# Kernel optimization log

Hardware: AMD Instinct MI355X
Metric: run time of the kernel (lower is better)

The kernel has to match this reference:

```python
import jax, jax.numpy as jnp
import numpy as np

WIN = 8
HEADS = 8
DOWN = 4
STRIDE = WIN // DOWN  # 2
LEVELS = len([i for i in range(8) if WIN / DOWN**i >= 1])  # 2
EPS = 1e-5


def circular_pad(x, pad_r, pad_b):
    # x: (N, H, W, C) -> (N, H+pad_b, W+pad_r, C), circular repeat like torch repeat+slice
    N, H, W, C = x.shape
    Hr = -(-(H + pad_b) // H)
    Wr = -(-(W + pad_r) // W)
    return jnp.tile(x, (1, Hr, Wr, 1))[:, :H + pad_b, :W + pad_r, :]


def pad_fit_win(x, ws):
    N, H, W, C = x.shape
    H_ = -(-H // ws) * ws
    W_ = -(-W // ws) * ws
    return circular_pad(x, W_ - W, H_ - H)


def window_partition(x, ws):
    N, H, W, C = x.shape
    x = x.reshape(N, H // ws, ws, W // ws, ws, C)
    return x.transpose(0, 1, 3, 2, 4, 5).reshape(-1, ws, ws, C)


def window_reverse(w, ws, H, W):
    B = w.shape[0] // ((H // ws) * (W // ws))
    x = w.reshape(B, H // ws, W // ws, ws, ws, -1)
    return x.transpose(0, 1, 3, 2, 4, 5).reshape(B, H, W, -1)


def layernorm(x, g, b):
    mu = jnp.mean(x, -1, keepdims=True)
    var = jnp.var(x, -1, keepdims=True)
    return (x - mu) * jax.lax.rsqrt(var + EPS) * g + b


def mha(q, k, v, wq, wk, wv, wf, bf):
    # q: (B, Lq, C); k, v: (B, Lk, C). Weights stored as (in, out); eval mode (no dropout).
    B, Lq, C = q.shape
    Lk = k.shape[1]
    dh = C // HEADS
    qh = (q @ wq).reshape(B, Lq, HEADS, dh)
    kh = (k @ wk).reshape(B, Lk, HEADS, dh)
    vh = (v @ wv).reshape(B, Lk, HEADS, dh)
    attn = jnp.einsum('bqhd,bkhd->bhqk', qh, kh) * (1.0 / dh ** 0.5)
    attn = jax.nn.softmax(attn, axis=-1)
    o = jnp.einsum('bhqk,bkhd->bqhd', attn, vh).reshape(B, Lq, C)
    return o @ wf + bf


def self_attention(x, wq, wk, wv, wf, bf):
    N, H, W, C = x.shape
    xp = pad_fit_win(x, WIN)
    _, H_, W_, _ = xp.shape
    xw = window_partition(xp, WIN).reshape(-1, WIN * WIN, C)
    res = mha(xw, xw, xw, wq, wk, wv, wf, bf)
    res = window_reverse(res.reshape(-1, WIN, WIN, C), WIN, H_, W_)
    return (xp + res)[:, :H, :W, :]


def cross_attention(q, kv, wq, wk, wv, wf, bf):
    # q: (N,qH,qW,C) non-overlapping windows; kv: (N,kH,kW,C) overlapping unfold windows
    N, qH, qW, C = q.shape
    _, kH, kW, _ = kv.shape
    qp = pad_fit_win(q, WIN)
    _, qH_, qW_, _ = qp.shape
    qw = window_partition(qp, WIN).reshape(-1, WIN * WIN, C)
    kH_ = (-(-kH // STRIDE) - 1) * STRIDE + WIN
    kW_ = (-(-kW // STRIDE) - 1) * STRIDE + WIN
    kvp = circular_pad(kv, kW_ - kW, kH_ - kH)
    nH = (kH_ - WIN) // STRIDE + 1
    nW = (kW_ - WIN) // STRIDE + 1
    ri = (jnp.arange(nH) * STRIDE)[:, None] + jnp.arange(WIN)
    ci = (jnp.arange(nW) * STRIDE)[:, None] + jnp.arange(WIN)
    patches = kvp[:, ri][:, :, :, ci]
    patches = patches.transpose(0, 1, 3, 2, 4, 5).reshape(-1, WIN * WIN, C)
    res = mha(qw, patches, patches, wq, wk, wv, wf, bf)
    res = window_reverse(res.reshape(-1, WIN, WIN, C), WIN, qH_, qW_)
    return (qp + res)[:, :qH, :qW, :]


def avgpool4(x):  # NHWC avg pool with kernel=stride=DOWN
    N, H, W, C = x.shape
    return x.reshape(N, H // DOWN, DOWN, W // DOWN, DOWN, C).mean((2, 4))


def setup_inputs() -> dict:
    key = jax.random.key(0)
    ks = jax.random.split(key, 12)
    D, DF = 256, 1024
    N, H, W = 8, 128, 128
    s = 0.02

    def w(k, shape):
        return jax.random.normal(k, shape, jnp.float32) * s

    return {
        'x': jax.random.normal(ks[0], (N, D, H, W), jnp.float32),
        'sa_wq': w(ks[1], (D, D)), 'sa_wk': w(ks[2], (D, D)), 'sa_wv': w(ks[3], (D, D)),
        'sa_wf': w(ks[4], (D, D)), 'sa_bf': jnp.zeros((D,), jnp.float32),
        'ca_wq': w(ks[5], (D, D)), 'ca_wk': w(ks[6], (D, D)), 'ca_wv': w(ks[7], (D, D)),
        'ca_wf': w(ks[8], (D, D)), 'ca_bf': jnp.zeros((D,), jnp.float32),
        'ln_self_g': jnp.ones((D,), jnp.float32), 'ln_self_b': jnp.zeros((D,), jnp.float32),
        'ln_cross_g': jnp.ones((D,), jnp.float32), 'ln_cross_b': jnp.zeros((D,), jnp.float32),
        'ffn_w1': w(ks[9], (D, DF)), 'ffn_b1': jnp.zeros((DF,), jnp.float32),
        'ffn_w2': w(ks[10], (DF, D)), 'ffn_b2': jnp.zeros((D,), jnp.float32),
        'ln_out_g': jnp.ones((D,), jnp.float32), 'ln_out_b': jnp.zeros((D,), jnp.float32),
    }


def reference(x, sa_wq, sa_wk, sa_wv, sa_wf, sa_bf,
              ca_wq, ca_wk, ca_wv, ca_wf, ca_bf,
              ln_self_g, ln_self_b, ln_cross_g, ln_cross_b,
              ffn_w1, ffn_b1, ffn_w2, ffn_b2, ln_out_g, ln_out_b):
    N, C, H, W = x.shape
    xh = x.transpose(0, 2, 3, 1)  # NHWC
    xh = pad_fit_win(xh, WIN)
    attn_list = []
    for idx in range(LEVELS):
        xa = self_attention(xh, sa_wq, sa_wk, sa_wv, sa_wf, sa_bf)
        xa = layernorm(xa, ln_self_g, ln_self_b)
        attn_list.append(xa)
        if idx < LEVELS - 1:
            xh = avgpool4(xa)
    kv = attn_list[-1]
    for idx in range(LEVELS - 1, 0, -1):
        q = cross_attention(attn_list[idx - 1], kv, ca_wq, ca_wk, ca_wv, ca_wf, ca_bf)
        q = layernorm(q, ln_cross_g, ln_cross_b)
        kv = q
    q = kv[:, :H, :W, :]
    res = jax.nn.relu(q @ ffn_w1 + ffn_b1) @ ffn_w2 + ffn_b2
    out = layernorm(q + res, ln_out_g, ln_out_b)
    return out.transpose(0, 3, 1, 2)
```

## Files before the change

kernel.cpp:

```cpp
#include <hip/hip_runtime.h>

typedef _Float16 h16;
typedef _Float16 f16x8 __attribute__((ext_vector_type(8)));
typedef _Float16 f16x4 __attribute__((ext_vector_type(4)));
typedef float f32x4 __attribute__((ext_vector_type(4)));

__device__ __forceinline__ float b2f(h16 v){ return (float)v; }
__device__ __forceinline__ h16 f2b(float v){ return (h16)v; }

#define CDIM 256
#define NHEADS 8
#define DH 32

__global__ __launch_bounds__(256) void k_wt_all(const float* __restrict__ s0, const float* __restrict__ s1,
                                                const float* __restrict__ s2, const float* __restrict__ s3,
                                                const float* __restrict__ s4, const float* __restrict__ s5,
                                                const float* __restrict__ s6, const float* __restrict__ s7,
                                                const float* __restrict__ s8, const float* __restrict__ s9,
                                                h16* __restrict__ wsc)
{
    __shared__ float T[32][33];
    int b = blockIdx.x;
    const float* src; h16* dst; int K, N, ti, tj;
    if (b < 512) {
        int w = b >> 6, rem = b & 63;
        ti = rem >> 3; tj = rem & 7; K = 256; N = 256;
        switch (w) {
            case 0: src = s0; break; case 1: src = s1; break;
            case 2: src = s2; break; case 3: src = s3; break;
            case 4: src = s4; break; case 5: src = s5; break;
            case 6: src = s6; break; default: src = s7; break;
        }
        dst = wsc + w * 65536;
    } else if (b < 768) {
        int rem = b - 512; ti = rem >> 5; tj = rem & 31; K = 256; N = 1024;
        src = s8; dst = wsc + 8 * 65536;
    } else {
        int rem = b - 768; ti = rem >> 3; tj = rem & 7; K = 1024; N = 256;
        src = s9; dst = wsc + 8 * 65536 + 262144;
    }
    int rr = threadIdx.x >> 5, c = threadIdx.x & 31;
    #pragma unroll
    for (int i = 0; i < 4; ++i) {
        int r = i * 8 + rr;
        T[r][c] = src[(long long)(ti * 32 + r) * N + tj * 32 + c];
    }
    __syncthreads();
    #pragma unroll
    for (int i = 0; i < 4; ++i) {
        int r = i * 8 + rr;
        dst[(long long)(tj * 32 + r) * K + ti * 32 + c] = f2b(T[c][r]);
    }
}

__global__ __launch_bounds__(256) void k_nchw2nhwc(const float* __restrict__ x, h16* __restrict__ o,
                                                   int Hh, int Ww)
{
    __shared__ float T[64][65];
    int bid = blockIdx.x;
    int cb = bid & 3; bid >>= 2;
    int nwb = Ww >> 6;
    int wb = bid % nwb; bid /= nwb;
    int h = bid % Hh;
    int n = bid / Hh;
    int lane = threadIdx.x & 63, grp = threadIdx.x >> 6;
    int w0 = wb << 6;
    long long HW = (long long)Hh * Ww;
    long long rbase = ((long long)(n * CDIM + cb * 64) * Hh + h) * Ww + w0;
    #pragma unroll
    for (int i = 0; i < 16; ++i) {
        int cl = grp * 16 + i;
        T[cl][lane] = x[rbase + (long long)cl * HW + lane];
    }
    __syncthreads();
    long long obase = (long long)(n * Hh + h) * Ww + w0;
    #pragma unroll
    for (int i = 0; i < 16; ++i) {
        int wl = grp * 16 + i;
        o[(obase + wl) * CDIM + cb * 64 + lane] = f2b(T[lane][wl]);
    }
}

__global__ __launch_bounds__(256) void k_gemm_mfma(const h16* __restrict__ A, const h16* __restrict__ Bt,
                                                   const float* __restrict__ bias, const h16* __restrict__ Cadd,
                                                   h16* __restrict__ C,
                                                   int M, int N, int K, int ldbt, int ldc,
                                                   long long ostride, int relu)
{
    __shared__ __align__(16) h16 As[128 * 64];
    __shared__ __align__(16) h16 Bs[128 * 64];
    const int tid = threadIdx.x;
    const int wave = tid >> 6, lane = tid & 63;
    const int row0 = blockIdx.y * 128, col0 = blockIdx.x * 128;
    const int wm = (wave >> 1) * 64, wn = (wave & 1) * 64;

    f32x4 acc[4][4] = {};

    const int srow = wave * 32 + (lane >> 3);
    const int skel = (lane & 7) * 8;
    const h16* ag = A  + (long long)(row0 + srow) * K    + skel;
    const h16* bg = Bt + (long long)(col0 + srow) * ldbt + skel;
    h16* as_base = As + (wave * 32) * 64;
    h16* bs_base = Bs + (wave * 32) * 64;

    for (int k0 = 0; k0 < K; k0 += 64) {
        #pragma unroll
        for (int i = 0; i < 4; ++i) {
            __builtin_amdgcn_global_load_lds(
                (const __attribute__((address_space(1))) void*)(ag + (long long)i * 8 * K),
                (__attribute__((address_space(3))) void*)(as_base + i * 8 * 64), 16, 0, 0);
            __builtin_amdgcn_global_load_lds(
                (const __attribute__((address_space(1))) void*)(bg + (long long)i * 8 * ldbt),
                (__attribute__((address_space(3))) void*)(bs_base + i * 8 * 64), 16, 0, 0);
        }
        ag += 64; bg += 64;
        __syncthreads();
        #pragma unroll
        for (int kk = 0; kk < 2; ++kk) {
            const int ko = kk * 32 + (lane >> 4) * 8;
            f16x8 af[4], bb[4];
            #pragma unroll
            for (int i = 0; i < 4; ++i) {
                af[i] = *(const f16x8*)(As + (wm + i * 16 + (lane & 15)) * 64 + ko);
                bb[i] = *(const f16x8*)(Bs + (wn + i * 16 + (lane & 15)) * 64 + ko);
            }
            #pragma unroll
            for (int i = 0; i < 4; ++i)
                #pragma unroll
                for (int j = 0; j < 4; ++j)
                    acc[i][j] = __builtin_amdgcn_mfma_f32_16x16x32_f16(af[i], bb[j], acc[i][j], 0, 0, 0);
        }
        __syncthreads();
    }

    const int cr = (lane >> 4) * 4;
    const int cc = lane & 15;
    #pragma unroll
    for (int j = 0; j < 4; ++j) {
        int col = col0 + wn + j * 16 + cc;
        int grp = col >> 8;
        long long cb = (long long)grp * ostride + (col & 255);
        float bv = bias ? bias[col] : 0.f;
        #pragma unroll
        for (int i = 0; i < 4; ++i) {
            #pragma unroll
            for (int r = 0; r < 4; ++r) {
                long long row = row0 + wm + i * 16 + cr + r;
                float v = acc[i][j][r] + bv;
                if (relu) v = fmaxf(v, 0.f);
                long long addr = cb + row * ldc;
                if (Cadd) v += b2f(Cadd[addr]);
                C[addr] = f2b(v);
            }
        }
    }
}

__global__ __launch_bounds__(256) void k_attn_mfma(const h16* __restrict__ Q, const h16* __restrict__ Kp,
                                                   const h16* __restrict__ Vp, h16* __restrict__ O,
                                                   int Hh, int Ww, int cross)
{
    __shared__ __align__(16) h16 SpA[4][64 * 64];
    __shared__ __align__(16) h16 VtA[4][32 * 64];
    const int tid = threadIdx.x;
    const int wave = tid >> 6, lane = tid & 63;
    const int l15 = lane & 15, g = lane >> 4;
    h16* Sp = SpA[wave];
    h16* Vt = VtA[wave];

    const int win = blockIdx.x;
    int n, wi, wj;
    if (cross) { n = win >> 8; wi = (win >> 4) & 15; wj = win & 15; }
    else {
        int nw = Ww >> 3, nh = Hh >> 3;
        n = win / (nh * nw);
        int rem = win - n * (nh * nw);
        wi = rem / nw; wj = rem - (rem / nw) * nw;
    }
    auto qtok = [&](int t) {
        return cross ? (n * 128 + wi * 8 + (t >> 3)) * 128 + wj * 8 + (t & 7)
                     : (n * Hh + wi * 8 + (t >> 3)) * Ww + wj * 8 + (t & 7);
    };
    auto ktok = [&](int t) {
        return cross ? (n * 32 + ((wi * 2 + (t >> 3)) & 31)) * 32 + ((wj * 2 + (t & 7)) & 31)
                     : qtok(t);
    };
    const float scale = 0.17677669529663687f;

    int qt_frag[4], kt_frag[4];
    #pragma unroll
    for (int i = 0; i < 4; ++i) { qt_frag[i] = qtok(i * 16 + l15); kt_frag[i] = ktok(i * 16 + l15); }
    const int vtok = ktok(lane);
    int otok[4][4];
    #pragma unroll
    for (int qt = 0; qt < 4; ++qt)
        #pragma unroll
        for (int rr = 0; rr < 4; ++rr)
            otok[qt][rr] = qtok(qt * 16 + g * 4 + rr);

    #pragma unroll 1
    for (int hh = 0; hh < 2; ++hh) {
        const int h = wave * 2 + hh;
        const int hoff = h * 32;

        f16x8 vin[4];
        #pragma unroll
        for (int j = 0; j < 4; ++j)
            vin[j] = *(const f16x8*)(Vp + (long long)vtok * CDIM + hoff + j * 8);

        f16x8 kf[4], qf[4];
        #pragma unroll
        for (int i = 0; i < 4; ++i) {
            kf[i] = *(const f16x8*)(Kp + (long long)kt_frag[i] * CDIM + hoff + g * 8);
            qf[i] = *(const f16x8*)(Q  + (long long)qt_frag[i] * CDIM + hoff + g * 8);
        }

        #pragma unroll
        for (int j = 0; j < 4; ++j)
            #pragma unroll
            for (int e = 0; e < 8; ++e) {
                int d = j * 8 + e;
                Vt[(d * 64 + lane) ^ ((d & 7) << 3)] = vin[j][e];
            }

        f32x4 sT[4][4] = {};
        #pragma unroll
        for (int i = 0; i < 4; ++i)
            #pragma unroll
            for (int jq = 0; jq < 4; ++jq)
                sT[i][jq] = __builtin_amdgcn_mfma_f32_16x16x32_f16(kf[i], qf[jq], sT[i][jq], 0, 0, 0);

        #pragma unroll
        for (int jq = 0; jq < 4; ++jq) {
            float m = -1e30f;
            #pragma unroll
            for (int i = 0; i < 4; ++i)
                #pragma unroll
                for (int rr = 0; rr < 4; ++rr)
                    m = fmaxf(m, sT[i][jq][rr]);
            m = fmaxf(m, __shfl_xor(m, 16));
            m = fmaxf(m, __shfl_xor(m, 32));
            float p[16];
            float sum = 0.f;
            #pragma unroll
            for (int i = 0; i < 4; ++i)
                #pragma unroll
                for (int rr = 0; rr < 4; ++rr) {
                    float e = __expf((sT[i][jq][rr] - m) * scale);
                    p[i * 4 + rr] = e; sum += e;
                }
            sum += __shfl_xor(sum, 16);
            sum += __shfl_xor(sum, 32);
            float inv = 1.f / sum;
            int q = jq * 16 + l15;
            int rowbase = q * 64, swz = (q & 7) << 3;
            #pragma unroll
            for (int i = 0; i < 4; ++i) {
                f16x4 pk;
                pk[0] = (h16)(p[i * 4 + 0] * inv);
                pk[1] = (h16)(p[i * 4 + 1] * inv);
                pk[2] = (h16)(p[i * 4 + 2] * inv);
                pk[3] = (h16)(p[i * 4 + 3] * inv);
                *(f16x4*)(Sp + ((rowbase + i * 16 + g * 4) ^ swz)) = pk;
            }
        }
        asm volatile("s_waitcnt lgkmcnt(0)" ::: "memory");

        f32x4 o[4][2] = {};
        #pragma unroll
        for (int kb = 0; kb < 2; ++kb) {
            f16x8 vb[2];
            #pragma unroll
            for (int dt = 0; dt < 2; ++dt) {
                int d = dt * 16 + l15;
                vb[dt] = *(const f16x8*)(Vt + ((d * 64 + kb * 32 + g * 8) ^ ((d & 7) << 3)));
            }
            #pragma unroll
            for (int qt = 0; qt < 4; ++qt) {
                int q = qt * 16 + l15;
                f16x8 pa = *(const f16x8*)(Sp + ((q * 64 + kb * 32 + g * 8) ^ ((q & 7) << 3)));
                #pragma unroll
                for (int dt = 0; dt < 2; ++dt)
                    o[qt][dt] = __builtin_amdgcn_mfma_f32_16x16x32_f16(pa, vb[dt], o[qt][dt], 0, 0, 0);
            }
        }

        #pragma unroll
        for (int qt = 0; qt < 4; ++qt)
            #pragma unroll
            for (int rr = 0; rr < 4; ++rr) {
                long long tb = (long long)otok[qt][rr] * CDIM + hoff;
                #pragma unroll
                for (int dt = 0; dt < 2; ++dt)
                    O[tb + dt * 16 + l15] = f2b(o[qt][dt][rr]);
            }
        asm volatile("s_waitcnt lgkmcnt(0)" ::: "memory");
    }
}

__global__ __launch_bounds__(256) void k_ln(const h16* __restrict__ A, const h16* __restrict__ Bb,
                                            const float* __restrict__ g, const float* __restrict__ be,
                                            h16* __restrict__ O)
{
    int tid = threadIdx.x;
    int t = tid >> 5;
    int j = tid & 31;
    long long base = ((long long)blockIdx.x * 8 + t) * CDIM + j * 8;
    f16x8 a = *(const f16x8*)(A + base);
    f16x8 b = *(const f16x8*)(Bb + base);
    float v[8]; float s = 0.f, s2 = 0.f;
    #pragma unroll
    for (int e = 0; e < 8; ++e) { float vv = b2f(a[e]) + b2f(b[e]); v[e] = vv; s += vv; s2 += vv * vv; }
    #pragma unroll
    for (int off = 1; off < 32; off <<= 1) { s += __shfl_xor(s, off); s2 += __shfl_xor(s2, off); }
    float mu = s * (1.f / 256.f);
    float inv = rsqrtf(s2 * (1.f / 256.f) - mu * mu + 1e-5f);
    f32x4 g0 = *(const f32x4*)(g + j * 8),  g1 = *(const f32x4*)(g + j * 8 + 4);
    f32x4 e0 = *(const f32x4*)(be + j * 8), e1 = *(const f32x4*)(be + j * 8 + 4);
    f16x8 y;
    #pragma unroll
    for (int e = 0; e < 4; ++e) y[e] = f2b((v[e] - mu) * inv * g0[e] + e0[e]);
    #pragma unroll
    for (int e = 0; e < 4; ++e) y[e + 4] = f2b((v[e + 4] - mu) * inv * g1[e] + e1[e]);
    *(f16x8*)(O + base) = y;
}

__global__ __launch_bounds__(256) void k_ln_out(const h16* __restrict__ A, const h16* __restrict__ Bb,
                                                const float* __restrict__ g, const float* __restrict__ be,
                                                float* __restrict__ O, int HW)
{
    __shared__ float Y[32][257];
    int tid = threadIdx.x;
    int t = tid >> 5;
    int j = tid & 31;
    long long tok0 = (long long)blockIdx.x * 32;
    f32x4 g0 = *(const f32x4*)(g + j * 8),  g1 = *(const f32x4*)(g + j * 8 + 4);
    f32x4 e0 = *(const f32x4*)(be + j * 8), e1 = *(const f32x4*)(be + j * 8 + 4);
    #pragma unroll
    for (int pass = 0; pass < 4; ++pass) {
        int ta = pass * 8 + t;
        long long base = (tok0 + ta) * CDIM + j * 8;
        f16x8 a = *(const f16x8*)(A + base);
        f16x8 b = *(const f16x8*)(Bb + base);
        float v[8]; float s = 0.f, s2 = 0.f;
        #pragma unroll
        for (int e = 0; e < 8; ++e) { float vv = b2f(a[e]) + b2f(b[e]); v[e] = vv; s += vv; s2 += vv * vv; }
        #pragma unroll
        for (int off = 1; off < 32; off <<= 1) { s += __shfl_xor(s, off); s2 += __shfl_xor(s2, off); }
        float mu = s * (1.f / 256.f);
        float inv = rsqrtf(s2 * (1.f / 256.f) - mu * mu + 1e-5f);
        #pragma unroll
        for (int e = 0; e < 4; ++e) Y[ta][j * 8 + e]     = (v[e] - mu) * inv * g0[e] + e0[e];
        #pragma unroll
        for (int e = 0; e < 4; ++e) Y[ta][j * 8 + 4 + e] = (v[e + 4] - mu) * inv * g1[e] + e1[e];
    }
    __syncthreads();
    int n = (int)(tok0 / HW);
    int hw0 = (int)(tok0 - (long long)n * HW);
    int tt = tid & 31;
    int cw = tid >> 5;
    #pragma unroll
    for (int k = 0; k < 32; ++k) {
        int c = k * 8 + cw;
        O[((long long)(n * CDIM + c)) * HW + hw0 + tt] = Y[tt][c];
    }
}

__global__ __launch_bounds__(256) void k_pool(const h16* __restrict__ A, h16* __restrict__ P,
                                              int Hin, int Win)
{
    int tok = blockIdx.x, c = threadIdx.x;
    int Wo = Win >> 2, Ho = Hin >> 2;
    int n = tok / (Ho * Wo);
    int rem = tok - n * (Ho * Wo);
    int i = rem / Wo, j = rem - (rem / Wo) * Wo;
    float s = 0.f;
    #pragma unroll
    for (int di = 0; di < 4; ++di)
        #pragma unroll
        for (int dj = 0; dj < 4; ++dj)
            s += b2f(A[(((long long)n * Hin + i * 4 + di) * Win + j * 4 + dj) * CDIM + c]);
    P[(long long)tok * CDIM + c] = f2b(s * 0.0625f);
}

extern "C" void kernel_launch(void* const* d_in, const int* in_sizes, int n_in,
                              void* d_out, int out_size, void* d_ws, size_t ws_size,
                              hipStream_t stream)
{
    const float* x     = (const float*)d_in[0];
    const float* sa_wq = (const float*)d_in[1];
    const float* sa_wk = (const float*)d_in[2];
    const float* sa_wv = (const float*)d_in[3];
    const float* sa_wf = (const float*)d_in[4];
    const float* sa_bf = (const float*)d_in[5];
    const float* ca_wq = (const float*)d_in[6];
    const float* ca_wk = (const float*)d_in[7];
    const float* ca_wv = (const float*)d_in[8];
    const float* ca_wf = (const float*)d_in[9];
    const float* ca_bf = (const float*)d_in[10];
    const float* lns_g = (const float*)d_in[11];
    const float* lns_b = (const float*)d_in[12];
    const float* lnc_g = (const float*)d_in[13];
    const float* lnc_b = (const float*)d_in[14];
    const float* w1    = (const float*)d_in[15];
    const float* b1    = (const float*)d_in[16];
    const float* w2    = (const float*)d_in[17];
    const float* b2    = (const float*)d_in[18];
    const float* lno_g = (const float*)d_in[19];
    const float* lno_b = (const float*)d_in[20];
    float* out = (float*)d_out;

    const int TOK0 = 8 * 128 * 128;
    const int TOK1 = 8 * 32 * 32;
    const size_t S0  = (size_t)TOK0 * CDIM * sizeof(h16);
    const size_t SML = (size_t)TOK1 * CDIM * sizeof(h16);
    char* ws = (char*)d_ws;
    h16* W0 = (h16*)(ws);
    h16* W1 = (h16*)(ws + S0);
    h16* W2 = (h16*)(ws + 2 * S0);
    h16* W3 = (h16*)(ws + 3 * S0);
    h16* P1 = (h16*)(ws + 0 * SML);
    h16* Q1 = (h16*)(ws + 1 * SML);
    h16* K1 = (h16*)(ws + 2 * SML);
    h16* V1 = (h16*)(ws + 3 * SML);
    h16* J1 = (h16*)(ws + 4 * SML);
    h16* A1 = (h16*)(ws + 5 * SML);
    h16* Kc = (h16*)(ws + 6 * SML);
    h16* Vc = (h16*)(ws + 7 * SML);

    const size_t WSC_BYTES = (8 * 65536 + 262144 + 262144) * sizeof(h16);
    h16* wsc;
    if (ws_size >= 4 * S0 + WSC_BYTES)
        wsc = (h16*)(ws + 4 * S0);
    else
        wsc = (h16*)d_out;
    h16* sa_wqT = wsc + 0 * 65536;
    h16* sa_wfT = wsc + 3 * 65536;
    h16* ca_wqT = wsc + 4 * 65536;
    h16* ca_wkT = wsc + 5 * 65536;
    h16* ca_wfT = wsc + 7 * 65536;
    h16* w1T    = wsc + 8 * 65536;
    h16* w2T    = wsc + 8 * 65536 + 262144;

    const long long OS0 = (long long)TOK0 * CDIM;
    const long long OS1 = (long long)TOK1 * CDIM;

    dim3 blk(256);
    dim3 gQKV0(6, TOK0 / 128), gP0(2, TOK0 / 128);
    dim3 gQKV1(6, TOK1 / 128), gP1(2, TOK1 / 128);
    dim3 gKV(4, TOK1 / 128);
    dim3 gF1(4, TOK0 / 128), gF2(2, TOK0 / 128);

    k_wt_all<<<1024, blk, 0, stream>>>(sa_wq, sa_wk, sa_wv, sa_wf, ca_wq, ca_wk, ca_wv, ca_wf,
                                       w1, w2, wsc);

    k_nchw2nhwc<<<8 * 128 * 2 * 4, blk, 0, stream>>>(x, W0, 128, 128);
    k_gemm_mfma<<<gQKV0, blk, 0, stream>>>(W0, sa_wqT, nullptr, nullptr, W1, TOK0, 768, 256, 256, 256, OS0, 0);
    k_attn_mfma<<<TOK0 / 64, blk, 0, stream>>>(W1, W2, W3, W1, 128, 128, 0);
    k_gemm_mfma<<<gP0, blk, 0, stream>>>(W1, sa_wfT, sa_bf, nullptr, W2, TOK0, 256, 256, 256, 256, 0, 0);
    k_ln<<<TOK0 / 8, blk, 0, stream>>>(W0, W2, lns_g, lns_b, W3);

    k_pool<<<TOK1, blk, 0, stream>>>(W3, P1, 128, 128);
    k_gemm_mfma<<<gQKV1, blk, 0, stream>>>(P1, sa_wqT, nullptr, nullptr, Q1, TOK1, 768, 256, 256, 256, OS1, 0);
    k_attn_mfma<<<TOK1 / 64, blk, 0, stream>>>(Q1, K1, V1, Q1, 32, 32, 0);
    k_gemm_mfma<<<gP1, blk, 0, stream>>>(Q1, sa_wfT, sa_bf, nullptr, J1, TOK1, 256, 256, 256, 256, 0, 0);
    k_ln<<<TOK1 / 8, blk, 0, stream>>>(P1, J1, lns_g, lns_b, A1);

    k_gemm_mfma<<<gP0, blk, 0, stream>>>(W3, ca_wqT, nullptr, nullptr, W1, TOK0, 256, 256, 256, 256, 0, 0);
    k_gemm_mfma<<<gKV, blk, 0, stream>>>(A1, ca_wkT, nullptr, nullptr, Kc, TOK1, 512, 256, 256, 256, OS1, 0);
    k_attn_mfma<<<TOK0 / 64, blk, 0, stream>>>(W1, Kc, Vc, W1, 0, 0, 1);
    k_gemm_mfma<<<gP0, blk, 0, stream>>>(W1, ca_wfT, ca_bf, nullptr, W2, TOK0, 256, 256, 256, 256, 0, 0);
    k_ln<<<TOK0 / 8, blk, 0, stream>>>(W3, W2, lnc_g, lnc_b, W1);

    k_gemm_mfma<<<gF1, blk, 0, stream>>>(W1, w1T,             b1,       nullptr, W2, TOK0, 512, 256, 256, 512, 256, 1);
    k_gemm_mfma<<<gF2, blk, 0, stream>>>(W2, w2T,             b2,       nullptr, W0, TOK0, 256, 512, 1024, 256, 0, 0);
    k_gemm_mfma<<<gF1, blk, 0, stream>>>(W1, w1T + 512 * 256, b1 + 512, nullptr, W2, TOK0, 512, 256, 256, 512, 256, 1);
    k_gemm_mfma<<<gF2, blk, 0, stream>>>(W2, w2T + 512,       nullptr,  W0,      W0, TOK0, 256, 512, 1024, 256, 0, 0);
    k_ln_out<<<TOK0 / 32, blk, 0, stream>>>(W1, W0, lno_g, lno_b, out, 128 * 128);
}
```

Baseline: 1.169 ms.

## Fuse output-projection GEMMs with residual LayerNorm, swizzle LDS, remap workgroups

Adds a 512-thread GEMM kernel that computes a full 256-wide row tile, then applies bias, residual add and LayerNorm in the epilogue. This replaces the separate projection GEMM plus LN kernel pairs, and the final FFN GEMM plus output LN when workspace allows. The aim is to drop intermediate round trips to global memory and some kernel launches. The generic GEMM also gains an XOR swizzle on LDS chunks to cut bank conflicts and a workgroup index remap intended to improve cache locality. In exchange, each fused block holds more LDS and registers, which may lower occupancy.

New measurement: 1.156 ms. Within noise of the previous version (-1.1%).

```diff
diff --git a/kernel.cpp b/kernel.cpp
--- a/kernel.cpp
+++ b/kernel.cpp
@@ -84,22 +84,30 @@
 __global__ __launch_bounds__(256) void k_gemm_mfma(const h16* __restrict__ A, const h16* __restrict__ Bt,
                                                    const float* __restrict__ bias, const h16* __restrict__ Cadd,
                                                    h16* __restrict__ C,
-                                                   int M, int N, int K, int ldbt, int ldc,
+                                                   int N, int K, int ldA, int ldbt, int ldc,
                                                    long long ostride, int relu)
 {
     __shared__ __align__(16) h16 As[128 * 64];
     __shared__ __align__(16) h16 Bs[128 * 64];
     const int tid = threadIdx.x;
     const int wave = tid >> 6, lane = tid & 63;
-    const int row0 = blockIdx.y * 128, col0 = blockIdx.x * 128;
+    const int l15 = lane & 15, g = lane >> 4;
+    const int gx = gridDim.x;
+    int L = blockIdx.y * gx + blockIdx.x;
+    const int nwg = gx * gridDim.y;
+    if ((nwg & 7) == 0) {
+        const int cpx = nwg >> 3;
+        L = (L & 7) * cpx + (L >> 3);
+    }
+    const int row0 = (L / gx) * 128, col0 = (L % gx) * 128;
     const int wm = (wave >> 1) * 64, wn = (wave & 1) * 64;
 
     f32x4 acc[4][4] = {};
 
     const int srow = wave * 32 + (lane >> 3);
-    const int skel = (lane & 7) * 8;
-    const h16* ag = A  + (long long)(row0 + srow) * K    + skel;
-    const h16* bg = Bt + (long long)(col0 + srow) * ldbt + skel;
+    const int sch  = ((lane & 7) ^ (srow & 7)) * 8;
+    const h16* ag = A  + (long long)(row0 + srow) * ldA  + sch;
+    const h16* bg = Bt + (long long)(col0 + srow) * ldbt + sch;
     h16* as_base = As + (wave * 32) * 64;
     h16* bs_base = Bs + (wave * 32) * 64;
 
@@ -107,7 +115,7 @@
         #pragma unroll
         for (int i = 0; i < 4; ++i) {
             __builtin_amdgcn_global_load_lds(
-                (const __attribute__((address_space(1))) void*)(ag + (long long)i * 8 * K),
+                (const __attribute__((address_space(1))) void*)(ag + (long long)i * 8 * ldA),
                 (__attribute__((address_space(3))) void*)(as_base + i * 8 * 64), 16, 0, 0);
             __builtin_amdgcn_global_load_lds(
                 (const __attribute__((address_space(1))) void*)(bg + (long long)i * 8 * ldbt),
@@ -117,12 +125,13 @@
         __syncthreads();
         #pragma unroll
         for (int kk = 0; kk < 2; ++kk) {
-            const int ko = kk * 32 + (lane >> 4) * 8;
+            const int c = kk * 4 + g;
+            const int slot = (c ^ (l15 & 7)) << 3;
             f16x8 af[4], bb[4];
             #pragma unroll
             for (int i = 0; i < 4; ++i) {
-                af[i] = *(const f16x8*)(As + (wm + i * 16 + (lane & 15)) * 64 + ko);
-                bb[i] = *(const f16x8*)(Bs + (wn + i * 16 + (lane & 15)) * 64 + ko);
+                af[i] = *(const f16x8*)(As + (wm + i * 16 + l15) * 64 + slot);
+                bb[i] = *(const f16x8*)(Bs + (wn + i * 16 + l15) * 64 + slot);
             }
             #pragma unroll
             for (int i = 0; i < 4; ++i)
@@ -133,11 +142,10 @@
         __syncthreads();
     }
 
-    const int cr = (lane >> 4) * 4;
-    const int cc = lane & 15;
+    const int cr = g * 4;
     #pragma unroll
     for (int j = 0; j < 4; ++j) {
-        int col = col0 + wn + j * 16 + cc;
+        int col = col0 + wn + j * 16 + l15;
         int grp = col >> 8;
         long long cb = (long long)grp * ostride + (col & 255);
         float bv = bias ? bias[col] : 0.f;
@@ -151,6 +159,149 @@
                 long long addr = cb + row * ldc;
                 if (Cadd) v += b2f(Cadd[addr]);
                 C[addr] = f2b(v);
+            }
+        }
+    }
+}
+
+__global__ __launch_bounds__(512) void k_gemm_ln(const h16* __restrict__ A, const h16* __restrict__ Bt,
+                                                 const float* __restrict__ bias, const h16* __restrict__ Cadd,
+                                                 const h16* __restrict__ R,
+                                                 const float* __restrict__ gw, const float* __restrict__ bw,
+                                                 h16* __restrict__ O16, float* __restrict__ O32,
+                                                 int K, int ldA, int ldbt, int HW, int mode)
+{
+    __shared__ __align__(16) h16 As[128 * 64];
+    __shared__ __align__(16) h16 Bs[256 * 64];
+    __shared__ float red[2][128][4];
+    const int tid = threadIdx.x;
+    const int wave = tid >> 6, lane = tid & 63;
+    const int l15 = lane & 15, g = lane >> 4;
+    const int row0 = blockIdx.x * 128;
+    const int wm = (wave >> 2) * 64, wn = (wave & 3) * 64;
+
+    f32x4 acc[4][4] = {};
+
+    const int ar = wave * 16 + (lane >> 3);
+    const int br = wave * 32 + (lane >> 3);
+    const int ach = ((lane & 7) ^ (ar & 7)) * 8;
+    const int bch = ((lane & 7) ^ (br & 7)) * 8;
+    const h16* ag = A  + (long long)(row0 + ar) * ldA + ach;
+    const h16* bg = Bt + (long long)br * ldbt + bch;
+    h16* as_base = As + (wave * 16) * 64;
+    h16* bs_base = Bs + (wave * 32) * 64;
+
+    for (int k0 = 0; k0 < K; k0 += 64) {
+        #pragma unroll
+        for (int i = 0; i < 2; ++i)
+            __builtin_amdgcn_global_load_lds(
+                (const __attribute__((address_space(1))) void*)(ag + (long long)i * 8 * ldA),
+                (__attribute__((address_space(3))) void*)(as_base + i * 8 * 64), 16, 0, 0);
+        #pragma unroll
+        for (int i = 0; i < 4; ++i)
+            __builtin_amdgcn_global_load_lds(
+                (const __attribute__((address_space(1))) void*)(bg + (long long)i * 8 * ldbt),
+                (__attribute__((address_space(3))) void*)(bs_base + i * 8 * 64), 16, 0, 0);
+        ag += 64; bg += 64;
+        __syncthreads();
+        #pragma unroll
+        for (int kk = 0; kk < 2; ++kk) {
+            const int c = kk * 4 + g;
+            const int slot = (c ^ (l15 & 7)) << 3;
+            f16x8 af[4], bb[4];
+            #pragma unroll
+            for (int i = 0; i < 4; ++i) {
+                af[i] = *(const f16x8*)(As + (wm + i * 16 + l15) * 64 + slot);
+                bb[i] = *(const f16x8*)(Bs + (wn + i * 16 + l15) * 64 + slot);
+            }
+            #pragma unroll
+            for (int i = 0; i < 4; ++i)
+                #pragma unroll
+                for (int j = 0; j < 4; ++j)
+                    acc[i][j] = __builtin_amdgcn_mfma_f32_16x16x32_f16(af[i], bb[j], acc[i][j], 0, 0, 0);
+        }
+        __syncthreads();
+    }
+
+    float sr[4][4] = {}, sr2[4][4] = {};
+    #pragma unroll
+    for (int j = 0; j < 4; ++j) {
+        int col = wn + j * 16 + l15;
+        float bv = bias ? bias[col] : 0.f;
+        #pragma unroll
+        for (int i = 0; i < 4; ++i) {
+            #pragma unroll
+            for (int r = 0; r < 4; ++r) {
+                long long row = row0 + wm + i * 16 + g * 4 + r;
+                float u = acc[i][j][r] + bv;
+                if (Cadd) u += b2f(Cadd[row * CDIM + col]);
+                u += b2f(R[row * CDIM + col]);
+                acc[i][j][r] = u;
+                sr[i][r] += u; sr2[i][r] += u * u;
+            }
+        }
+    }
+    #pragma unroll
+    for (int i = 0; i < 4; ++i)
+        #pragma unroll
+        for (int r = 0; r < 4; ++r) {
+            float s = sr[i][r], s2 = sr2[i][r];
+            #pragma unroll
+            for (int off = 1; off < 16; off <<= 1) { s += __shfl_xor(s, off); s2 += __shfl_xor(s2, off); }
+            sr[i][r] = s; sr2[i][r] = s2;
+        }
+    if (l15 == 0) {
+        #pragma unroll
+        for (int i = 0; i < 4; ++i)
+            #pragma unroll
+            for (int r = 0; r < 4; ++r) {
+                int lr = wm + i * 16 + g * 4 + r;
+                red[0][lr][wave & 3] = sr[i][r];
+                red[1][lr][wave & 3] = sr2[i][r];
+            }
+    }
+    __syncthreads();
+    float mu_[4][4], iv_[4][4];
+    #pragma unroll
+    for (int i = 0; i < 4; ++i)
+        #pragma unroll
+        for (int r = 0; r < 4; ++r) {
+            int lr = wm + i * 16 + g * 4 + r;
+            f32x4 p = *(const f32x4*)&red[0][lr][0];
+            f32x4 q = *(const f32x4*)&red[1][lr][0];
+            float ts  = p[0] + p[1] + p[2] + p[3];
+            float ts2 = q[0] + q[1] + q[2] + q[3];
+            float mu = ts * (1.f / 256.f);
+            mu_[i][r] = mu;
+            iv_[i][r] = rsqrtf(ts2 * (1.f / 256.f) - mu * mu + 1e-5f);
+        }
+    if (mode == 0) {
+        #pragma unroll
+        for (int j = 0; j < 4; ++j) {
+            int col = wn + j * 16 + l15;
+            float gc = gw[col], bc = bw[col];
+            #pragma unroll
+            for (int i = 0; i < 4; ++i)
+                #pragma unroll
+                for (int r = 0; r < 4; ++r) {
+                    long long row = row0 + wm + i * 16 + g * 4 + r;
+                    O16[row * CDIM + col] = f2b((acc[i][j][r] - mu_[i][r]) * iv_[i][r] * gc + bc);
+                }
+        }
+    } else {
+        #pragma unroll
+        for (int j = 0; j < 4; ++j) {
+            int col = wn + j * 16 + l15;
+            float gc = gw[col], bc = bw[col];
+            #pragma unroll
+            for (int i = 0; i < 4; ++i) {
+                int tok0 = row0 + wm + i * 16 + g * 4;
+                int n = tok0 / HW, hw = tok0 - n * HW;
+                f32x4 y;
+                #pragma unroll
+                for (int r = 0; r < 4; ++r)
+                    y[r] = (acc[i][j][r] - mu_[i][r]) * iv_[i][r] * gc + bc;
+                *(f32x4*)(O32 + (long long)(n * CDIM + col) * HW + hw) = y;
             }
         }
     }
@@ -296,33 +447,6 @@
             }
         asm volatile("s_waitcnt lgkmcnt(0)" ::: "memory");
     }
-}
-
-__global__ __launch_bounds__(256) void k_ln(const h16* __restrict__ A, const h16* __restrict__ Bb,
-                                            const float* __restrict__ g, const float* __restrict__ be,
-                                            h16* __restrict__ O)
-{
-    int tid = threadIdx.x;
-    int t = tid >> 5;
-    int j = tid & 31;
-    long long base = ((long long)blockIdx.x * 8 + t) * CDIM + j * 8;
-    f16x8 a = *(const f16x8*)(A + base);
-    f16x8 b = *(const f16x8*)(Bb + base);
-    float v[8]; float s = 0.f, s2 = 0.f;
-    #pragma unroll
-    for (int e = 0; e < 8; ++e) { float vv = b2f(a[e]) + b2f(b[e]); v[e] = vv; s += vv; s2 += vv * vv; }
-    #pragma unroll
-    for (int off = 1; off < 32; off <<= 1) { s += __shfl_xor(s, off); s2 += __shfl_xor(s2, off); }
-    float mu = s * (1.f / 256.f);
-    float inv = rsqrtf(s2 * (1.f / 256.f) - mu * mu + 1e-5f);
-    f32x4 g0 = *(const f32x4*)(g + j * 8),  g1 = *(const f32x4*)(g + j * 8 + 4);
-    f32x4 e0 = *(const f32x4*)(be + j * 8), e1 = *(const f32x4*)(be + j * 8 + 4);
-    f16x8 y;
-    #pragma unroll
-    for (int e = 0; e < 4; ++e) y[e] = f2b((v[e] - mu) * inv * g0[e] + e0[e]);
-    #pragma unroll
-    for (int e = 0; e < 4; ++e) y[e + 4] = f2b((v[e + 4] - mu) * inv * g1[e] + e1[e]);
-    *(f16x8*)(O + base) = y;
 }
 
 __global__ __launch_bounds__(256) void k_ln_out(const h16* __restrict__ A, const h16* __restrict__ Bb,
@@ -419,21 +543,18 @@
     h16* W1 = (h16*)(ws + S0);
     h16* W2 = (h16*)(ws + 2 * S0);
     h16* W3 = (h16*)(ws + 3 * S0);
+    h16* H  = W2;
     h16* P1 = (h16*)(ws + 0 * SML);
     h16* Q1 = (h16*)(ws + 1 * SML);
     h16* K1 = (h16*)(ws + 2 * SML);
     h16* V1 = (h16*)(ws + 3 * SML);
-    h16* J1 = (h16*)(ws + 4 * SML);
     h16* A1 = (h16*)(ws + 5 * SML);
     h16* Kc = (h16*)(ws + 6 * SML);
     h16* Vc = (h16*)(ws + 7 * SML);
 
     const size_t WSC_BYTES = (8 * 65536 + 262144 + 262144) * sizeof(h16);
-    h16* wsc;
-    if (ws_size >= 4 * S0 + WSC_BYTES)
-        wsc = (h16*)(ws + 4 * S0);
-    else
-        wsc = (h16*)d_out;
+    bool tailws = ws_size >= 4 * S0 + WSC_BYTES;
+    h16* wsc = tailws ? (h16*)(ws + 4 * S0) : (h16*)d_out;
     h16* sa_wqT = wsc + 0 * 65536;
     h16* sa_wfT = wsc + 3 * 65536;
     h16* ca_wqT = wsc + 4 * 65536;
@@ -445,36 +566,37 @@
     const long long OS0 = (long long)TOK0 * CDIM;
     const long long OS1 = (long long)TOK1 * CDIM;
 
-    dim3 blk(256);
-    dim3 gQKV0(6, TOK0 / 128), gP0(2, TOK0 / 128);
-    dim3 gQKV1(6, TOK1 / 128), gP1(2, TOK1 / 128);
-    dim3 gKV(4, TOK1 / 128);
-    dim3 gF1(4, TOK0 / 128), gF2(2, TOK0 / 128);
+    dim3 blk(256), blk2(512);
 
     k_wt_all<<<1024, blk, 0, stream>>>(sa_wq, sa_wk, sa_wv, sa_wf, ca_wq, ca_wk, ca_wv, ca_wf,
                                        w1, w2, wsc);
 
     k_nchw2nhwc<<<8 * 128 * 2 * 4, blk, 0, stream>>>(x, W0, 128, 128);
-    k_gemm_mfma<<<gQKV0, blk, 0, stream>>>(W0, sa_wqT, nullptr, nullptr, W1, TOK0, 768, 256, 256, 256, OS0, 0);
+    k_gemm_mfma<<<dim3(6, TOK0 / 128), blk, 0, stream>>>(W0, sa_wqT, nullptr, nullptr, W1, 768, 256, 256, 256, 256, OS0, 0);
     k_attn_mfma<<<TOK0 / 64, blk, 0, stream>>>(W1, W2, W3, W1, 128, 128, 0);
-    k_gemm_mfma<<<gP0, blk, 0, stream>>>(W1, sa_wfT, sa_bf, nullptr, W2, TOK0, 256, 256, 256, 256, 0, 0);
-    k_ln<<<TOK0 / 8, blk, 0, stream>>>(W0, W2, lns_g, lns_b, W3);
+    k_gemm_ln<<<TOK0 / 128, blk2, 0, stream>>>(W1, sa_wfT, sa_bf, nullptr, W0, lns_g, lns_b,
+                                               W3, nullptr, 256, 256, 256, 16384, 0);
 
     k_pool<<<TOK1, blk, 0, stream>>>(W3, P1, 128, 128);
-    k_gemm_mfma<<<gQKV1, blk, 0, stream>>>(P1, sa_wqT, nullptr, nullptr, Q1, TOK1, 768, 256, 256, 256, OS1, 0);
+    k_gemm_mfma<<<dim3(6, TOK1 / 128), blk, 0, stream>>>(P1, sa_wqT, nullptr, nullptr, Q1, 768, 256, 256, 256, 256, OS1, 0);
     k_attn_mfma<<<TOK1 / 64, blk, 0, stream>>>(Q1, K1, V1, Q1, 32, 32, 0);
-    k_gemm_mfma<<<gP1, blk, 0, stream>>>(Q1, sa_wfT, sa_bf, nullptr, J1, TOK1, 256, 256, 256, 256, 0, 0);
-    k_ln<<<TOK1 / 8, blk, 0, stream>>>(P1, J1, lns_g, lns_b, A1);
-
-    k_gemm_mfma<<<gP0, blk, 0, stream>>>(W3, ca_wqT, nullptr, nullptr, W1, TOK0, 256, 256, 256, 256, 0, 0);
-    k_gemm_mfma<<<gKV, blk, 0, stream>>>(A1, ca_wkT, nullptr, nullptr, Kc, TOK1, 512, 256, 256, 256, OS1, 0);
+    k_gemm_ln<<<TOK1 / 128, blk2, 0, stream>>>(Q1, sa_wfT, sa_bf, nullptr, P1, lns_g, lns_b,
+                                               A1, nullptr, 256, 256, 256, 1024, 0);
+
+    k_gemm_mfma<<<dim3(2, TOK0 / 128), blk, 0, stream>>>(W3, ca_wqT, nullptr, nullptr, W1, 256, 256, 256, 256, 256, 0, 0);
+    k_gemm_mfma<<<dim3(4, TOK1 / 128), blk, 0, stream>>>(A1, ca_wkT, nullptr, nullptr, Kc, 512, 256, 256, 256, 256, OS1, 0);
     k_attn_mfma<<<TOK0 / 64, blk, 0, stream>>>(W1, Kc, Vc, W1, 0, 0, 1);
-    k_gemm_mfma<<<gP0, blk, 0, stream>>>(W1, ca_wfT, ca_bf, nullptr, W2, TOK0, 256, 256, 256, 256, 0, 0);
-    k_ln<<<TOK0 / 8, blk, 0, stream>>>(W3, W2, lnc_g, lnc_b, W1);
-
-    k_gemm_mfma<<<gF1, blk, 0, stream>>>(W1, w1T,             b1,       nullptr, W2, TOK0, 512, 256, 256, 512, 256, 1);
-    k_gemm_mfma<<<gF2, blk, 0, stream>>>(W2, w2T,             b2,       nullptr, W0, TOK0, 256, 512, 1024, 256, 0, 0);
-    k_gemm_mfma<<<gF1, blk, 0, stream>>>(W1, w1T + 512 * 256, b1 + 512, nullptr, W2, TOK0, 512, 256, 256, 512, 256, 1);
-    k_gemm_mfma<<<gF2, blk, 0, stream>>>(W2, w2T + 512,       nullptr,  W0,      W0, TOK0, 256, 512, 1024, 256, 0, 0);
-    k_ln_out<<<TOK0 / 32, blk, 0, stream>>>(W1, W0, lno_g, lno_b, out, 128 * 128);
-}
+    k_gemm_ln<<<TOK0 / 128, blk2, 0, stream>>>(W1, ca_wfT, ca_bf, nullptr, W3, lnc_g, lnc_b,
+                                               W1, nullptr, 256, 256, 256, 16384, 0);
+
+    k_gemm_mfma<<<dim3(4, TOK0 / 128), blk, 0, stream>>>(W1, w1T,             b1,       nullptr, H,  512, 256, 256, 256, 512, 256, 1);
+    k_gemm_mfma<<<dim3(2, TOK0 / 128), blk, 0, stream>>>(H,  w2T,             b2,       nullptr, W0, 256, 512, 512, 1024, 256, 0, 0);
+    k_gemm_mfma<<<dim3(4, TOK0 / 128), blk, 0, stream>>>(W1, w1T + 512 * 256, b1 + 512, nullptr, H,  512, 256, 256, 256, 512, 256, 1);
+    if (tailws) {
+        k_gemm_ln<<<TOK0 / 128, blk2, 0, stream>>>(H, w2T + 512, nullptr, W0, W1, lno_g, lno_b,
+                                                   nullptr, out, 512, 512, 1024, 16384, 1);
+    } else {
+        k_gemm_mfma<<<dim3(2, TOK0 / 128), blk, 0, stream>>>(H, w2T + 512, nullptr, W0, W0, 256, 512, 512, 1024, 256, 0, 0);
+        k_ln_out<<<TOK0 / 32, blk, 0, stream>>>(W1, W0, lno_g, lno_b, out, 16384);
+    }
+}
```
